# Kernel tuning notes

Measured on AMD Instinct MI355X. Metric: run time of the kernel, lower is better.

Reference implementation:

```python
import jax, jax.numpy as jnp
import numpy as np

B, S, HIDDEN = 2, 2048, 2048
HEADS, GROUPS, KVC = 16, 4, 128
HPG = HEADS // GROUPS  # heads per group
LAYER_INDEX = 2
SOFTMAX_SCALE = KVC ** -0.5
ROPE_THETA = 10000.0


def _rope_tables(seq_len, dim, dtype=jnp.float32):
    inv_freq = 1.0 / (ROPE_THETA ** (jnp.arange(0, dim, 2, dtype=jnp.float32) / dim))
    t = jnp.arange(seq_len, dtype=jnp.float32)
    freqs = jnp.outer(t, inv_freq)  # [S, dim/2]
    return jnp.cos(freqs).astype(dtype), jnp.sin(freqs).astype(dtype)


def _apply_rope(x, cos, sin):
    # x: [b, s, h, d]; rotate-half (GPT-NeoX style)
    d2 = x.shape[-1] // 2
    x1, x2 = x[..., :d2], x[..., d2:]
    c = cos[None, :, None, :]
    s = sin[None, :, None, :]
    return jnp.concatenate([x1 * c - x2 * s, x2 * c + x1 * s], axis=-1)


def setup_inputs() -> dict:
    key = jax.random.key(0)
    k1, k2, k3, k4 = jax.random.split(key, 4)
    std = HIDDEN ** -0.5
    return {
        "x": jax.random.normal(k1, (B, S, HIDDEN), dtype=jnp.float32),
        "w_q": jax.random.normal(k2, (HIDDEN, HEADS * KVC), dtype=jnp.float32) * std,
        "w_kv": jax.random.normal(k3, (HIDDEN, 2 * GROUPS * KVC), dtype=jnp.float32) * std,
        "w_dense": jax.random.normal(k4, (HEADS * KVC, HIDDEN), dtype=jnp.float32) * std,
    }


def reference(x, w_q, w_kv, w_dense):
    b, s, _ = x.shape
    # QKV projections
    q = (x @ w_q).reshape(b, s, HEADS, KVC)                 # [b,s,H,d]
    kv = (x @ w_kv).reshape(b, s, 2, GROUPS, KVC)
    k, v = kv[:, :, 0], kv[:, :, 1]                          # [b,s,G,d]
    # Rotary embeddings on q and k
    cos, sin = _rope_tables(s, KVC, x.dtype)
    q = _apply_rope(q, cos, sin)
    k = _apply_rope(k, cos, sin)
    # GQA attention with per-layer scaling trick:
    # scores computed at scale/softmax of layer_index, cast fp32, rescaled back.
    qg = q.reshape(b, s, GROUPS, HPG, KVC)
    scores = jnp.einsum("bqghd,bkgd->bghqk", qg, k) * (SOFTMAX_SCALE / LAYER_INDEX)
    scores = scores.astype(jnp.float32) * LAYER_INDEX
    # causal mask
    causal = jnp.tril(jnp.ones((s, s), dtype=bool))
    mask_value = jnp.finfo(jnp.float32).min
    scores = jnp.where(causal[None, None, None, :, :], scores, mask_value)
    probs = jax.nn.softmax(scores, axis=-1).astype(x.dtype)  # dropout p=0 (eval)
    ctx = jnp.einsum("bghqk,bkgd->bqghd", probs, v).reshape(b, s, HEADS * KVC)
    return ctx @ w_dense
```

## Files before the change

kernel.cpp:

```cpp
#include <hip/hip_runtime.h>
#include <hip/hip_bf16.h>
#include <stdint.h>

typedef unsigned short u16;
typedef __bf16 bf16x8 __attribute__((ext_vector_type(8)));
typedef float f32x4 __attribute__((ext_vector_type(4)));

#define S_LEN 2048
#define BATCH 2
#define NHEADS 16
#define NGROUPS 4
#define DHEAD 128
#define QKV_W 3072

__device__ __forceinline__ float bf2f(u16 u) {
  union { uint32_t i; float f; } v; v.i = ((uint32_t)u) << 16; return v.f;
}
__device__ __forceinline__ u16 f2bf(float f) {
  union { float f; uint32_t i; } v; v.f = f;
  uint32_t r = v.i + 0x7FFF + ((v.i >> 16) & 1);
  return (u16)(r >> 16);
}
__device__ __forceinline__ void llds16(const void* g, void* l) {
  __builtin_amdgcn_global_load_lds(
      (const __attribute__((address_space(1))) uint32_t*)g,
      (__attribute__((address_space(3))) uint32_t*)l, 16, 0, 0);
}

__device__ __forceinline__ void store_out(u16* C, long i, float v) { C[i] = f2bf(v); }
__device__ __forceinline__ void store_out(float* C, long i, float v) { C[i] = v; }

__global__ void rope_tables_k(float* __restrict__ cosT, float* __restrict__ sinT) {
  int i = blockIdx.x * 256 + threadIdx.x;
  int s = i >> 6, j = i & 63;
  float inv = exp2f(-(float)j * 0.20762050593045983f);
  float ang = (float)s * inv;
  float sv, cv;
  sincosf(ang, &sv, &cv);
  cosT[i] = cv; sinT[i] = sv;
}

__global__ void cvt_f32_bf16(const float* __restrict__ in, u16* __restrict__ out) {
  long i = ((long)blockIdx.x * 256 + threadIdx.x) * 4;
  float4 v = *(const float4*)(in + i);
  ushort4 o;
  o.x = f2bf(v.x); o.y = f2bf(v.y); o.z = f2bf(v.z); o.w = f2bf(v.w);
  *(ushort4*)(out + i) = o;
}

__global__ void transpose_f32_bf16(const float* __restrict__ in, u16* __restrict__ out,
                                   int R, int C) {
  __shared__ u16 tile[32][33];
  int c0 = blockIdx.x * 32, r0 = blockIdx.y * 32;
  int tx = threadIdx.x, ty = threadIdx.y;
  for (int i = 0; i < 32; i += 8)
    tile[ty + i][tx] = f2bf(in[(long)(r0 + ty + i) * C + c0 + tx]);
  __syncthreads();
  for (int i = 0; i < 32; i += 8)
    out[(long)(c0 + ty + i) * R + r0 + tx] = tile[tx][ty + i];
}

#define GFENCE() asm volatile("" ::: "memory")
#define MIDBAR() do { GFENCE(); __builtin_amdgcn_s_barrier(); \
    asm volatile("s_waitcnt lgkmcnt(0)" ::: "memory"); } while (0)
#define ENDBAR() do { GFENCE(); __builtin_amdgcn_s_barrier(); GFENCE(); } while (0)

__device__ __forceinline__ bf16x8 frag_ld(const __bf16* h, int wrow, int kk, int quad) {
  int b = ((wrow & 15) << 6) | (quad << 4);
  b ^= ((wrow >> 3) & 1) << 5;
  int off = ((((wrow >> 4) << 1) | kk) << 10) | b;
  return *(const bf16x8*)((const char*)h + off);
}

__device__ __forceinline__ void stage_half(const u16* __restrict__ g, int K,
                                           __bf16* lhalf, int wv, int lane) {
  int bsrc = (lane << 4) ^ (((lane >> 5) & 1) << 5);
  int r = bsrc >> 6, c = (bsrc & 63) >> 1;
  int cb = (wv & 1) << 5;
  llds16(g + (long)((wv >> 1) * 16 + r) * K + cb + c,
         lhalf + wv * 512 + lane * 8);
  llds16(g + (long)((4 + (wv >> 1)) * 16 + r) * K + cb + c,
         lhalf + 4096 + wv * 512 + lane * 8);
}

template <typename OutT>
__global__ __launch_bounds__(512) void gemm_bt8(
    const u16* __restrict__ A, const u16* __restrict__ Bt, OutT* __restrict__ C,
    int M, int N, int K) {
  __shared__ __align__(16) __bf16 lds[2][2][16384];
  const int tid = threadIdx.x;
  const int wv = tid >> 6, lane = tid & 63;
  const int quad = lane >> 4, l16 = lane & 15;
  const int wr = wv >> 2, wc = wv & 3;

  const int nwg = gridDim.x * gridDim.y;
  const int orig = blockIdx.y * gridDim.x + blockIdx.x;
  const int swz = (orig & 7) * (nwg >> 3) + (orig >> 3);
  const int bx = swz % gridDim.x, by = swz / gridDim.x;
  const int bm = by * 256, bn = bx * 256;

  const u16* Abase = A + (long)bm * K;
  const u16* Bbase = Bt + (long)bn * K;
  const int NT = K >> 6;

  f32x4 acc[8][4] = {};

  stage_half(Abase, K, &lds[0][0][0], wv, lane);
  stage_half(Abase + (long)128 * K, K, &lds[0][0][8192], wv, lane);
  stage_half(Bbase, K, &lds[0][1][0], wv, lane);
  stage_half(Bbase + (long)128 * K, K, &lds[0][1][8192], wv, lane);
  stage_half(Abase + 64, K, &lds[1][0][0], wv, lane);
  stage_half(Abase + (long)128 * K + 64, K, &lds[1][0][8192], wv, lane);
  stage_half(Bbase + 64, K, &lds[1][1][0], wv, lane);
  stage_half(Bbase + (long)128 * K + 64, K, &lds[1][1][8192], wv, lane);
  asm volatile("s_waitcnt vmcnt(8)" ::: "memory");
  __builtin_amdgcn_s_barrier();
  GFENCE();

  for (int kt = 0; kt < NT; ++kt) {
    const int buf = kt & 1;
    const __bf16* Ah = &lds[buf][0][wr * 8192];
    const __bf16* Bh = &lds[buf][1][(wc >> 1) * 8192];
    const int brow0 = (wc & 1) << 6;
    const bool pre = (kt + 2 < NT);
    bf16x8 aF[4][2], bF[4][2];

#pragma unroll
    for (int m = 0; m < 4; ++m) {
      aF[m][0] = frag_ld(Ah, m * 16 + l16, 0, quad);
      aF[m][1] = frag_ld(Ah, m * 16 + l16, 1, quad);
    }
#pragma unroll
    for (int n = 0; n < 2; ++n) {
      bF[n][0] = frag_ld(Bh, brow0 + n * 16 + l16, 0, quad);
      bF[n][1] = frag_ld(Bh, brow0 + n * 16 + l16, 1, quad);
    }
    MIDBAR();
    __builtin_amdgcn_s_setprio(1);
#pragma unroll
    for (int m = 0; m < 4; ++m)
#pragma unroll
      for (int n = 0; n < 2; ++n) {
        acc[m][n] = __builtin_amdgcn_mfma_f32_16x16x32_bf16(aF[m][0], bF[n][0], acc[m][n], 0, 0, 0);
        acc[m][n] = __builtin_amdgcn_mfma_f32_16x16x32_bf16(aF[m][1], bF[n][1], acc[m][n], 0, 0, 0);
      }
    __builtin_amdgcn_s_setprio(0);
    ENDBAR();

#pragma unroll
    for (int n = 2; n < 4; ++n) {
      bF[n][0] = frag_ld(Bh, brow0 + n * 16 + l16, 0, quad);
      bF[n][1] = frag_ld(Bh, brow0 + n * 16 + l16, 1, quad);
    }
    MIDBAR();
    __builtin_amdgcn_s_setprio(1);
#pragma unroll
    for (int m = 0; m < 4; ++m)
#pragma unroll
      for (int n = 2; n < 4; ++n) {
        acc[m][n] = __builtin_amdgcn_mfma_f32_16x16x32_bf16(aF[m][0], bF[n][0], acc[m][n], 0, 0, 0);
        acc[m][n] = __builtin_amdgcn_mfma_f32_16x16x32_bf16(aF[m][1], bF[n][1], acc[m][n], 0, 0, 0);
      }
    __builtin_amdgcn_s_setprio(0);
    ENDBAR();

#pragma unroll
    for (int m = 0; m < 4; ++m) {
      aF[m][0] = frag_ld(Ah, 64 + m * 16 + l16, 0, quad);
      aF[m][1] = frag_ld(Ah, 64 + m * 16 + l16, 1, quad);
    }
    if (pre) {
      const u16* p = Bbase + (long)(kt + 2) * 64;
      stage_half(p, K, &lds[buf][1][0], wv, lane);
      stage_half(p + (long)128 * K, K, &lds[buf][1][8192], wv, lane);
    }
    MIDBAR();
    __builtin_amdgcn_s_setprio(1);
#pragma unroll
    for (int m = 0; m < 4; ++m)
#pragma unroll
      for (int n = 2; n < 4; ++n) {
        acc[4 + m][n] = __builtin_amdgcn_mfma_f32_16x16x32_bf16(aF[m][0], bF[n][0], acc[4 + m][n], 0, 0, 0);
        acc[4 + m][n] = __builtin_amdgcn_mfma_f32_16x16x32_bf16(aF[m][1], bF[n][1], acc[4 + m][n], 0, 0, 0);
      }
    __builtin_amdgcn_s_setprio(0);
    ENDBAR();

    if (pre) {
      const u16* p = Abase + (long)(kt + 2) * 64;
      stage_half(p, K, &lds[buf][0][0], wv, lane);
      stage_half(p + (long)128 * K, K, &lds[buf][0][8192], wv, lane);
    }
    MIDBAR();
    __builtin_amdgcn_s_setprio(1);
#pragma unroll
    for (int m = 0; m < 4; ++m)
#pragma unroll
      for (int n = 0; n < 2; ++n) {
        acc[4 + m][n] = __builtin_amdgcn_mfma_f32_16x16x32_bf16(aF[m][0], bF[n][0], acc[4 + m][n], 0, 0, 0);
        acc[4 + m][n] = __builtin_amdgcn_mfma_f32_16x16x32_bf16(aF[m][1], bF[n][1], acc[4 + m][n], 0, 0, 0);
      }
    __builtin_amdgcn_s_setprio(0);
    if (pre) { asm volatile("s_waitcnt vmcnt(8)" ::: "memory"); }
    else     { asm volatile("s_waitcnt vmcnt(0)" ::: "memory"); }
    ENDBAR();
  }

  const long colbase = (long)bn + wc * 64 + l16;
#pragma unroll
  for (int mt = 0; mt < 8; ++mt)
#pragma unroll
    for (int nt = 0; nt < 4; ++nt)
#pragma unroll
      for (int rr = 0; rr < 4; ++rr) {
        long row = bm + wr * 128 + mt * 16 + quad * 4 + rr;
        store_out(C, row * N + colbase + nt * 16, acc[mt][nt][rr]);
      }
}

__global__ void rope_q_k(u16* __restrict__ qkv, const float* __restrict__ cosT,
                         const float* __restrict__ sinT) {
  long i = (long)blockIdx.x * 256 + threadIdx.x;
  int j = i & 63;
  long rest = i >> 6;
  int h = rest & 15;
  long bs = rest >> 4;
  int s = bs & (S_LEN - 1);
  long base = bs * QKV_W + h * DHEAD + j;
  float x1 = bf2f(qkv[base]), x2 = bf2f(qkv[base + 64]);
  float c = cosT[s * 64 + j], sn = sinT[s * 64 + j];
  qkv[base] = f2bf(x1 * c - x2 * sn);
  qkv[base + 64] = f2bf(x2 * c + x1 * sn);
}

__global__ void rope_k_k(const u16* __restrict__ qkv, u16* __restrict__ Kb,
                         const float* __restrict__ cosT, const float* __restrict__ sinT) {
  long i = (long)blockIdx.x * 256 + threadIdx.x;
  int j = i & 63;
  long rest = i >> 6;
  int g = rest & 3;
  long bs = rest >> 2;
  int s = bs & (S_LEN - 1);
  int b = (int)(bs >> 11);
  long src = bs * QKV_W + 2048 + g * 128 + j;
  float x1 = bf2f(qkv[src]), x2 = bf2f(qkv[src + 64]);
  float c = cosT[s * 64 + j], sn = sinT[s * 64 + j];
  long dst = ((long)(b * NGROUPS + g) * S_LEN + s) * DHEAD + j;
  Kb[dst] = f2bf(x1 * c - x2 * sn);
  Kb[dst + 64] = f2bf(x2 * c + x1 * sn);
}

__global__ void v_trans_k(const u16* __restrict__ qkv, u16* __restrict__ Vt) {
  __shared__ u16 tile[32][33];
  int s0 = blockIdx.x * 32, d0 = blockIdx.y * 32;
  int bg = blockIdx.z;
  int b = bg >> 2, g = bg & 3;
  int tx = threadIdx.x, ty = threadIdx.y;
  for (int i = 0; i < 32; i += 8) {
    long s = s0 + ty + i;
    tile[ty + i][tx] = qkv[((long)b * S_LEN + s) * QKV_W + 2560 + g * 128 + d0 + tx];
  }
  __syncthreads();
  for (int i = 0; i < 32; i += 8) {
    int d = d0 + ty + i;
    Vt[((long)(b * NGROUPS + g) * DHEAD + d) * S_LEN + s0 + tx] = tile[tx][ty + i];
  }
}

__global__ __launch_bounds__(512, 2) void attn_k8(
    const u16* __restrict__ Q,
    const u16* __restrict__ Kb,
    const u16* __restrict__ Vt,
    u16* __restrict__ ctx) {
  __shared__ __align__(16) __bf16 Ks[2][64 * 128];
  __shared__ __align__(16) __bf16 Vts[2][128 * 64];
  __shared__ __align__(16) __bf16 Ps[256 * 64];

  const int h = blockIdx.y, b = blockIdx.z, g = h >> 2;
  const int tile = blockIdx.x;
  const int q0 = tile * 256;
  const int nch = 4 * (tile + 1);

  const int tid = threadIdx.x, wv = tid >> 6, lane = tid & 63;
  const int quad = lane >> 4, l16 = lane & 15;
  const float SCALE = 0.08838834764831845f;

  const long kbase = (long)(b * NGROUPS + g) * S_LEN * DHEAD;
  const long vbase = (long)(b * NGROUPS + g) * DHEAD * S_LEN;

  const int krow_off = lane >> 4;
  const int vrow_off = lane >> 3;

  const __bf16 oneb = (__bf16)((l16 == 0) ? 1.0f : 0.0f);
  const bf16x8 bones = {oneb, oneb, oneb, oneb, oneb, oneb, oneb, oneb};

  bf16x8 aq[2][4];
#pragma unroll
  for (int m = 0; m < 2; ++m) {
    const u16* qp = Q + (long)(b * S_LEN + q0 + wv * 32 + m * 16 + l16) * QKV_W + h * DHEAD + quad * 8;
#pragma unroll
    for (int ds = 0; ds < 4; ++ds)
      aq[m][ds] = *(const bf16x8*)(qp + ds * 32);
  }

#pragma unroll
  for (int i = 0; i < 2; ++i) {
    int r0 = wv * 8 + i * 4;
    int row = r0 + krow_off;
    int c = l16 ^ (row & 15);
    llds16(Kb + kbase + (long)row * DHEAD + c * 8, &Ks[0][r0 * 128 + lane * 8]);
  }
#pragma unroll
  for (int i = 0; i < 2; ++i) {
    int d0 = wv * 16 + i * 8;
    int row = d0 + vrow_off;
    int c = (lane & 7) ^ (row & 7);
    llds16(Vt + vbase + (long)row * S_LEN + c * 8, &Vts[0][d0 * 64 + lane * 8]);
  }
  __syncthreads();

  f32x4 Oacc[2][8] = {};
  f32x4 Osum[2] = {};
  const int rmin = q0 + wv * 32;

  for (int kc = 0; kc < nch; ++kc) {
    const int cur = kc & 1;
    if (kc + 1 < nch) {
      const int nxt = cur ^ 1;
#pragma unroll
      for (int i = 0; i < 2; ++i) {
        int r0 = wv * 8 + i * 4;
        int row = r0 + krow_off;
        int c = l16 ^ (row & 15);
        llds16(Kb + kbase + (long)((kc + 1) * 64 + row) * DHEAD + c * 8,
               &Ks[nxt][r0 * 128 + lane * 8]);
      }
#pragma unroll
      for (int i = 0; i < 2; ++i) {
        int d0 = wv * 16 + i * 8;
        int row = d0 + vrow_off;
        int c = (lane & 7) ^ (row & 7);
        llds16(Vt + vbase + (long)row * S_LEN + (kc + 1) * 64 + c * 8,
               &Vts[nxt][d0 * 64 + lane * 8]);
      }
    }

    const bool skip = (kc * 64) > (rmin + 31);
    if (!skip) {
      f32x4 sacc[2][4] = {};
      __builtin_amdgcn_s_setprio(1);
#pragma unroll
      for (int ds = 0; ds < 4; ++ds) {
        int pos0 = ((ds * 4 + quad) ^ l16) * 8;
#pragma unroll
        for (int nt = 0; nt < 4; ++nt) {
          bf16x8 bk = *(const bf16x8*)&Ks[cur][(nt * 16 + l16) * 128 + pos0];
          sacc[0][nt] = __builtin_amdgcn_mfma_f32_16x16x32_bf16(aq[0][ds], bk, sacc[0][nt], 0, 0, 0);
          sacc[1][nt] = __builtin_amdgcn_mfma_f32_16x16x32_bf16(aq[1][ds], bk, sacc[1][nt], 0, 0, 0);
        }
      }
      __builtin_amdgcn_s_setprio(0);

      const bool need_mask = (kc * 64 + 63) > rmin;
      if (need_mask) {
#pragma unroll
        for (int m = 0; m < 2; ++m)
#pragma unroll
          for (int nt = 0; nt < 4; ++nt)
#pragma unroll
            for (int r = 0; r < 4; ++r) {
              int qrow = rmin + m * 16 + quad * 4 + r;
              int key = kc * 64 + nt * 16 + l16;
              float p = (key <= qrow) ? __expf(sacc[m][nt][r] * SCALE) : 0.f;
              int qlocal = quad * 4 + r;
              int chunk = nt * 2 + (l16 >> 3);
              int pos = chunk ^ (qlocal & 7);
              Ps[(wv * 32 + m * 16 + qlocal) * 64 + pos * 8 + (l16 & 7)] = (__bf16)p;
            }
      } else {
#pragma unroll
        for (int m = 0; m < 2; ++m)
#pragma unroll
          for (int nt = 0; nt < 4; ++nt)
#pragma unroll
            for (int r = 0; r < 4; ++r) {
              float p = __expf(sacc[m][nt][r] * SCALE);
              int qlocal = quad * 4 + r;
              int chunk = nt * 2 + (l16 >> 3);
              int pos = chunk ^ (qlocal & 7);
              Ps[(wv * 32 + m * 16 + qlocal) * 64 + pos * 8 + (l16 & 7)] = (__bf16)p;
            }
      }

      bf16x8 ap[2][2];
#pragma unroll
      for (int m = 0; m < 2; ++m)
#pragma unroll
        for (int kf = 0; kf < 2; ++kf) {
          int pos = ((kf * 4 + quad) ^ (l16 & 7)) * 8;
          ap[m][kf] = *(const bf16x8*)&Ps[(wv * 32 + m * 16 + l16) * 64 + pos];
        }
      __builtin_amdgcn_s_setprio(1);
#pragma unroll
      for (int nt = 0; nt < 8; ++nt)
#pragma unroll
        for (int kf = 0; kf < 2; ++kf) {
          int pos = ((kf * 4 + quad) ^ (l16 & 7)) * 8;
          bf16x8 bv = *(const bf16x8*)&Vts[cur][(nt * 16 + l16) * 64 + pos];
          Oacc[0][nt] = __builtin_amdgcn_mfma_f32_16x16x32_bf16(ap[0][kf], bv, Oacc[0][nt], 0, 0, 0);
          Oacc[1][nt] = __builtin_amdgcn_mfma_f32_16x16x32_bf16(ap[1][kf], bv, Oacc[1][nt], 0, 0, 0);
        }
#pragma unroll
      for (int m = 0; m < 2; ++m) {
        Osum[m] = __builtin_amdgcn_mfma_f32_16x16x32_bf16(ap[m][0], bones, Osum[m], 0, 0, 0);
        Osum[m] = __builtin_amdgcn_mfma_f32_16x16x32_bf16(ap[m][1], bones, Osum[m], 0, 0, 0);
      }
      __builtin_amdgcn_s_setprio(0);
    }

    __syncthreads();
  }

#pragma unroll
  for (int m = 0; m < 2; ++m) {
    float lsum[4];
#pragma unroll
    for (int r = 0; r < 4; ++r)
      lsum[r] = __shfl(Osum[m][r], quad << 4, 64);

    const long obase = ((long)(b * S_LEN + q0 + wv * 32 + m * 16) * NHEADS + h) * DHEAD;
#pragma unroll
    for (int nt = 0; nt < 8; ++nt)
#pragma unroll
      for (int r = 0; r < 4; ++r) {
        int lrow = quad * 4 + r;
        ctx[obase + (long)lrow * NHEADS * DHEAD + nt * 16 + l16] =
            f2bf(Oacc[m][nt][r] / lsum[r]);
      }
  }
}

extern "C" void kernel_launch(void* const* d_in, const int* in_sizes, int n_in,
                              void* d_out, int out_size, void* d_ws, size_t ws_size,
                              hipStream_t stream) {
  const float* x   = (const float*)d_in[0];
  const float* wq  = (const float*)d_in[1];
  const float* wkv = (const float*)d_in[2];
  const float* wd  = (const float*)d_in[3];
  float* out = (float*)d_out;

  char* ws = (char*)d_ws;
  float* cosT  = (float*)(ws + 0);
  float* sinT  = (float*)(ws + 524288);
  u16* wqkvT = (u16*)(ws + 1048576);
  u16* wdT   = (u16*)(ws + 13631488);
  u16* xb    = (u16*)(ws + 22020096);
  u16* qkv   = (u16*)(ws + 38797312);
  u16* Kb    = (u16*)(ws + 63963136);
  u16* Vt    = (u16*)(ws + 68157440);
  u16* ctx   = (u16*)(ws + 72351744);

  rope_tables_k<<<512, 256, 0, stream>>>(cosT, sinT);
  cvt_f32_bf16<<<8192, 256, 0, stream>>>(x, xb);
  transpose_f32_bf16<<<dim3(64, 64), dim3(32, 8), 0, stream>>>(wq, wqkvT, 2048, 2048);
  transpose_f32_bf16<<<dim3(32, 64), dim3(32, 8), 0, stream>>>(wkv, wqkvT + (long)2048 * 2048, 2048, 1024);
  transpose_f32_bf16<<<dim3(64, 64), dim3(32, 8), 0, stream>>>(wd, wdT, 2048, 2048);

  gemm_bt8<u16><<<dim3(12, 16), 512, 0, stream>>>(xb, wqkvT, qkv, 4096, 3072, 2048);

  rope_q_k<<<16384, 256, 0, stream>>>(qkv, cosT, sinT);
  rope_k_k<<<4096, 256, 0, stream>>>(qkv, Kb, cosT, sinT);
  v_trans_k<<<dim3(64, 4, 8), dim3(32, 8), 0, stream>>>(qkv, Vt);

  attn_k8<<<dim3(8, 16, 2), 512, 0, stream>>>(qkv, Kb, Vt, ctx);

  gemm_bt8<float><<<dim3(8, 16), 512, 0, stream>>>(ctx, wdT, out, 4096, 2048, 2048);
}
```

Measured before the change: 343.5 us.

## Balance causal attention by pairing 128-row tiles and splitting keys across wave halves

```diff
diff --git a/kernel.cpp b/kernel.cpp
--- a/kernel.cpp
+++ b/kernel.cpp
@@ -267,22 +267,24 @@
   }
 }
 
-__global__ __launch_bounds__(512, 2) void attn_k8(
+__global__ __launch_bounds__(512, 2) void attn_k9(
     const u16* __restrict__ Q,
     const u16* __restrict__ Kb,
     const u16* __restrict__ Vt,
     u16* __restrict__ ctx) {
-  __shared__ __align__(16) __bf16 Ks[2][64 * 128];
-  __shared__ __align__(16) __bf16 Vts[2][128 * 64];
-  __shared__ __align__(16) __bf16 Ps[256 * 64];
+  __shared__ __align__(16) char smem[82432];
+  __bf16* Ks   = (__bf16*)smem;
+  __bf16* Vts  = (__bf16*)(smem + 32768);
+  __bf16* Ps   = (__bf16*)(smem + 65536);
+  float*  Psum = (float*)(smem + 81920);
+  float*  scr  = (float*)smem;
 
   const int h = blockIdx.y, b = blockIdx.z, g = h >> 2;
-  const int tile = blockIdx.x;
-  const int q0 = tile * 256;
-  const int nch = 4 * (tile + 1);
-
+  const int tx = blockIdx.x;
   const int tid = threadIdx.x, wv = tid >> 6, lane = tid & 63;
   const int quad = lane >> 4, l16 = lane & 15;
+  const int rg = wv & 3;
+  const int kh = wv >> 2;
   const float SCALE = 0.08838834764831845f;
 
   const long kbase = (long)(b * NGROUPS + g) * S_LEN * DHEAD;
@@ -294,149 +296,172 @@
   const __bf16 oneb = (__bf16)((l16 == 0) ? 1.0f : 0.0f);
   const bf16x8 bones = {oneb, oneb, oneb, oneb, oneb, oneb, oneb, oneb};
 
-  bf16x8 aq[2][4];
-#pragma unroll
-  for (int m = 0; m < 2; ++m) {
-    const u16* qp = Q + (long)(b * S_LEN + q0 + wv * 32 + m * 16 + l16) * QKV_W + h * DHEAD + quad * 8;
-#pragma unroll
-    for (int ds = 0; ds < 4; ++ds)
-      aq[m][ds] = *(const bf16x8*)(qp + ds * 32);
-  }
-
-#pragma unroll
-  for (int i = 0; i < 2; ++i) {
-    int r0 = wv * 8 + i * 4;
-    int row = r0 + krow_off;
-    int c = l16 ^ (row & 15);
-    llds16(Kb + kbase + (long)row * DHEAD + c * 8, &Ks[0][r0 * 128 + lane * 8]);
-  }
-#pragma unroll
-  for (int i = 0; i < 2; ++i) {
-    int d0 = wv * 16 + i * 8;
-    int row = d0 + vrow_off;
-    int c = (lane & 7) ^ (row & 7);
-    llds16(Vt + vbase + (long)row * S_LEN + c * 8, &Vts[0][d0 * 64 + lane * 8]);
-  }
-  __syncthreads();
-
-  f32x4 Oacc[2][8] = {};
-  f32x4 Osum[2] = {};
-  const int rmin = q0 + wv * 32;
-
-  for (int kc = 0; kc < nch; ++kc) {
-    const int cur = kc & 1;
-    if (kc + 1 < nch) {
-      const int nxt = cur ^ 1;
-#pragma unroll
-      for (int i = 0; i < 2; ++i) {
-        int r0 = wv * 8 + i * 4;
-        int row = r0 + krow_off;
-        int c = l16 ^ (row & 15);
-        llds16(Kb + kbase + (long)((kc + 1) * 64 + row) * DHEAD + c * 8,
-               &Ks[nxt][r0 * 128 + lane * 8]);
-      }
-#pragma unroll
-      for (int i = 0; i < 2; ++i) {
-        int d0 = wv * 16 + i * 8;
-        int row = d0 + vrow_off;
-        int c = (lane & 7) ^ (row & 7);
-        llds16(Vt + vbase + (long)row * S_LEN + (kc + 1) * 64 + c * 8,
-               &Vts[nxt][d0 * 64 + lane * 8]);
-      }
-    }
-
-    const bool skip = (kc * 64) > (rmin + 31);
-    if (!skip) {
-      f32x4 sacc[2][4] = {};
-      __builtin_amdgcn_s_setprio(1);
-#pragma unroll
-      for (int ds = 0; ds < 4; ++ds) {
-        int pos0 = ((ds * 4 + quad) ^ l16) * 8;
-#pragma unroll
-        for (int nt = 0; nt < 4; ++nt) {
-          bf16x8 bk = *(const bf16x8*)&Ks[cur][(nt * 16 + l16) * 128 + pos0];
-          sacc[0][nt] = __builtin_amdgcn_mfma_f32_16x16x32_bf16(aq[0][ds], bk, sacc[0][nt], 0, 0, 0);
-          sacc[1][nt] = __builtin_amdgcn_mfma_f32_16x16x32_bf16(aq[1][ds], bk, sacc[1][nt], 0, 0, 0);
+  __bf16* Pw = Ps + wv * 1024;
+
+  for (int pass = 0; pass < 2; ++pass) {
+    const int tile = pass ? (15 - tx) : tx;
+    const int q0 = tile * 128;
+    const int nch = 2 * (tile + 1);
+
+    bf16x8 aq[2][4];
+#pragma unroll
+    for (int m = 0; m < 2; ++m) {
+      const u16* qp = Q + (long)(b * S_LEN + q0 + rg * 32 + m * 16 + l16) * QKV_W + h * DHEAD + quad * 8;
+#pragma unroll
+      for (int ds = 0; ds < 4; ++ds)
+        aq[m][ds] = *(const bf16x8*)(qp + ds * 32);
+    }
+
+#pragma unroll
+    for (int i = 0; i < 2; ++i) {
+      int r0 = wv * 8 + i * 4;
+      int row = r0 + krow_off;
+      int c = l16 ^ (row & 15);
+      llds16(Kb + kbase + (long)row * DHEAD + c * 8, &Ks[r0 * 128 + lane * 8]);
+    }
+#pragma unroll
+    for (int i = 0; i < 2; ++i) {
+      int d0 = wv * 16 + i * 8;
+      int row = d0 + vrow_off;
+      int c = (lane & 7) ^ (row & 7);
+      llds16(Vt + vbase + (long)row * S_LEN + c * 8, &Vts[d0 * 64 + lane * 8]);
+    }
+    __syncthreads();
+
+    f32x4 Oacc[2][8] = {};
+    f32x4 Osum[2] = {};
+    const int rmin = q0 + rg * 32;
+
+    for (int kc = 0; kc < nch; ++kc) {
+      const int cur = kc & 1;
+      if (kc + 1 < nch) {
+        const int nxt = cur ^ 1;
+#pragma unroll
+        for (int i = 0; i < 2; ++i) {
+          int r0 = wv * 8 + i * 4;
+          int row = r0 + krow_off;
+          int c = l16 ^ (row & 15);
+          llds16(Kb + kbase + (long)((kc + 1) * 64 + row) * DHEAD + c * 8,
+                 &Ks[nxt * 8192 + r0 * 128 + lane * 8]);
         }
-      }
-      __builtin_amdgcn_s_setprio(0);
-
-      const bool need_mask = (kc * 64 + 63) > rmin;
-      if (need_mask) {
+#pragma unroll
+        for (int i = 0; i < 2; ++i) {
+          int d0 = wv * 16 + i * 8;
+          int row = d0 + vrow_off;
+          int c = (lane & 7) ^ (row & 7);
+          llds16(Vt + vbase + (long)row * S_LEN + (kc + 1) * 64 + c * 8,
+                 &Vts[nxt * 8192 + d0 * 64 + lane * 8]);
+        }
+      }
+
+      const int kb0 = kc * 64 + kh * 32;
+      const bool skip = kb0 > (rmin + 31);
+      if (!skip) {
+        f32x4 sacc[2][2] = {};
+        __builtin_amdgcn_s_setprio(1);
+#pragma unroll
+        for (int ds = 0; ds < 4; ++ds) {
+          int pos0 = ((ds * 4 + quad) ^ l16) * 8;
+#pragma unroll
+          for (int nt = 0; nt < 2; ++nt) {
+            bf16x8 bk = *(const bf16x8*)&Ks[cur * 8192 + (kh * 32 + nt * 16 + l16) * 128 + pos0];
+            sacc[0][nt] = __builtin_amdgcn_mfma_f32_16x16x32_bf16(aq[0][ds], bk, sacc[0][nt], 0, 0, 0);
+            sacc[1][nt] = __builtin_amdgcn_mfma_f32_16x16x32_bf16(aq[1][ds], bk, sacc[1][nt], 0, 0, 0);
+          }
+        }
+        __builtin_amdgcn_s_setprio(0);
+
+        const bool need_mask = (kb0 + 31) > rmin;
+        if (need_mask) {
+#pragma unroll
+          for (int m = 0; m < 2; ++m)
+#pragma unroll
+            for (int nt = 0; nt < 2; ++nt)
+#pragma unroll
+              for (int r = 0; r < 4; ++r) {
+                int qrow = rmin + m * 16 + quad * 4 + r;
+                int key = kb0 + nt * 16 + l16;
+                float p = (key <= qrow) ? __expf(sacc[m][nt][r] * SCALE) : 0.f;
+                int row = m * 16 + quad * 4 + r;
+                int gs = (nt * 2 + (l16 >> 3)) ^ quad;
+                Pw[row * 32 + gs * 8 + (l16 & 7)] = (__bf16)p;
+              }
+        } else {
+#pragma unroll
+          for (int m = 0; m < 2; ++m)
+#pragma unroll
+            for (int nt = 0; nt < 2; ++nt)
+#pragma unroll
+              for (int r = 0; r < 4; ++r) {
+                float p = __expf(sacc[m][nt][r] * SCALE);
+                int row = m * 16 + quad * 4 + r;
+                int gs = (nt * 2 + (l16 >> 3)) ^ quad;
+                Pw[row * 32 + gs * 8 + (l16 & 7)] = (__bf16)p;
+              }
+        }
+
+        bf16x8 ap[2];
+#pragma unroll
+        for (int m = 0; m < 2; ++m) {
+          int pos = (quad ^ ((l16 >> 2) & 3)) * 8;
+          ap[m] = *(const bf16x8*)&Pw[(m * 16 + l16) * 32 + pos];
+        }
+        __builtin_amdgcn_s_setprio(1);
+#pragma unroll
+        for (int nt = 0; nt < 8; ++nt) {
+          int pos = (((kh << 2) | quad) ^ (l16 & 7)) * 8;
+          bf16x8 bv = *(const bf16x8*)&Vts[cur * 8192 + (nt * 16 + l16) * 64 + pos];
+          Oacc[0][nt] = __builtin_amdgcn_mfma_f32_16x16x32_bf16(ap[0], bv, Oacc[0][nt], 0, 0, 0);
+          Oacc[1][nt] = __builtin_amdgcn_mfma_f32_16x16x32_bf16(ap[1], bv, Oacc[1][nt], 0, 0, 0);
+        }
 #pragma unroll
         for (int m = 0; m < 2; ++m)
-#pragma unroll
-          for (int nt = 0; nt < 4; ++nt)
-#pragma unroll
-            for (int r = 0; r < 4; ++r) {
-              int qrow = rmin + m * 16 + quad * 4 + r;
-              int key = kc * 64 + nt * 16 + l16;
-              float p = (key <= qrow) ? __expf(sacc[m][nt][r] * SCALE) : 0.f;
-              int qlocal = quad * 4 + r;
-              int chunk = nt * 2 + (l16 >> 3);
-              int pos = chunk ^ (qlocal & 7);
-              Ps[(wv * 32 + m * 16 + qlocal) * 64 + pos * 8 + (l16 & 7)] = (__bf16)p;
-            }
-      } else {
+          Osum[m] = __builtin_amdgcn_mfma_f32_16x16x32_bf16(ap[m], bones, Osum[m], 0, 0, 0);
+        __builtin_amdgcn_s_setprio(0);
+      }
+
+      __syncthreads();
+    }
+
+    if (kh == 1) {
+      float* s = scr + rg * 4096;
+#pragma unroll
+      for (int m = 0; m < 2; ++m)
+#pragma unroll
+        for (int nt = 0; nt < 8; ++nt)
+#pragma unroll
+          for (int r = 0; r < 4; ++r)
+            s[(m * 16 + quad * 4 + r) * 128 + nt * 16 + l16] = Oacc[m][nt][r];
+      if (l16 == 0) {
 #pragma unroll
         for (int m = 0; m < 2; ++m)
 #pragma unroll
-          for (int nt = 0; nt < 4; ++nt)
-#pragma unroll
-            for (int r = 0; r < 4; ++r) {
-              float p = __expf(sacc[m][nt][r] * SCALE);
-              int qlocal = quad * 4 + r;
-              int chunk = nt * 2 + (l16 >> 3);
-              int pos = chunk ^ (qlocal & 7);
-              Ps[(wv * 32 + m * 16 + qlocal) * 64 + pos * 8 + (l16 & 7)] = (__bf16)p;
-            }
-      }
-
-      bf16x8 ap[2][2];
-#pragma unroll
-      for (int m = 0; m < 2; ++m)
-#pragma unroll
-        for (int kf = 0; kf < 2; ++kf) {
-          int pos = ((kf * 4 + quad) ^ (l16 & 7)) * 8;
-          ap[m][kf] = *(const bf16x8*)&Ps[(wv * 32 + m * 16 + l16) * 64 + pos];
-        }
-      __builtin_amdgcn_s_setprio(1);
-#pragma unroll
-      for (int nt = 0; nt < 8; ++nt)
-#pragma unroll
-        for (int kf = 0; kf < 2; ++kf) {
-          int pos = ((kf * 4 + quad) ^ (l16 & 7)) * 8;
-          bf16x8 bv = *(const bf16x8*)&Vts[cur][(nt * 16 + l16) * 64 + pos];
-          Oacc[0][nt] = __builtin_amdgcn_mfma_f32_16x16x32_bf16(ap[0][kf], bv, Oacc[0][nt], 0, 0, 0);
-          Oacc[1][nt] = __builtin_amdgcn_mfma_f32_16x16x32_bf16(ap[1][kf], bv, Oacc[1][nt], 0, 0, 0);
-        }
+          for (int r = 0; r < 4; ++r)
+            Psum[rg * 32 + m * 16 + quad * 4 + r] = Osum[m][r];
+      }
+    }
+    __syncthreads();
+    if (kh == 0) {
+      float* s = scr + rg * 4096;
 #pragma unroll
       for (int m = 0; m < 2; ++m) {
-        Osum[m] = __builtin_amdgcn_mfma_f32_16x16x32_bf16(ap[m][0], bones, Osum[m], 0, 0, 0);
-        Osum[m] = __builtin_amdgcn_mfma_f32_16x16x32_bf16(ap[m][1], bones, Osum[m], 0, 0, 0);
-      }
-      __builtin_amdgcn_s_setprio(0);
-    }
-
+        float lsum[4];
+#pragma unroll
+        for (int r = 0; r < 4; ++r)
+          lsum[r] = __shfl(Osum[m][r], quad << 4, 64) +
+                    Psum[rg * 32 + m * 16 + quad * 4 + r];
+        const long obase = ((long)(b * S_LEN + q0 + rg * 32 + m * 16) * NHEADS + h) * DHEAD;
+#pragma unroll
+        for (int nt = 0; nt < 8; ++nt)
+#pragma unroll
+          for (int r = 0; r < 4; ++r) {
+            int lrow = quad * 4 + r;
+            float v = Oacc[m][nt][r] + s[(m * 16 + lrow) * 128 + nt * 16 + l16];
+            ctx[obase + (long)lrow * NHEADS * DHEAD + nt * 16 + l16] = f2bf(v / lsum[r]);
+          }
+      }
+    }
     __syncthreads();
-  }
-
-#pragma unroll
-  for (int m = 0; m < 2; ++m) {
-    float lsum[4];
-#pragma unroll
-    for (int r = 0; r < 4; ++r)
-      lsum[r] = __shfl(Osum[m][r], quad << 4, 64);
-
-    const long obase = ((long)(b * S_LEN + q0 + wv * 32 + m * 16) * NHEADS + h) * DHEAD;
-#pragma unroll
-    for (int nt = 0; nt < 8; ++nt)
-#pragma unroll
-      for (int r = 0; r < 4; ++r) {
-        int lrow = quad * 4 + r;
-        ctx[obase + (long)lrow * NHEADS * DHEAD + nt * 16 + l16] =
-            f2bf(Oacc[m][nt][r] / lsum[r]);
-      }
   }
 }
 
@@ -472,7 +497,7 @@
   rope_k_k<<<4096, 256, 0, stream>>>(qkv, Kb, cosT, sinT);
   v_trans_k<<<dim3(64, 4, 8), dim3(32, 8), 0, stream>>>(qkv, Vt);
 
-  attn_k8<<<dim3(8, 16, 2), 512, 0, stream>>>(qkv, Kb, Vt, ctx);
+  attn_k9<<<dim3(8, 16, 2), 512, 0, stream>>>(qkv, Kb, Vt, ctx);
 
   gemm_bt8<float><<<dim3(8, 16), 512, 0, stream>>>(ctx, wdT, out, 4096, 2048, 2048);
 }
```

Result: faster. 316.8 us (-7.8%).
